# Optimization experiments

Hardware: AMD Instinct MI355X
Metric: run time of the kernel (lower is better)

## Reference

```python
import jax, jax.numpy as jnp
import numpy as np

ITEM_NUM = 1_000_000
MAXLEN = 200
H = 128
NH = 2
NB = 2
B = 2048
FLOAT_MIN = -1000.0
EPS = 1e-8


def _ln(x, g, b):
    mu = jnp.mean(x, axis=-1, keepdims=True)
    var = jnp.mean((x - mu) ** 2, axis=-1, keepdims=True)
    return (x - mu) / jnp.sqrt(var + EPS) * g + b


def setup_inputs() -> dict:
    key = jax.random.key(0)
    ks = jax.random.split(key, 32)
    s = 1.0 / np.sqrt(H)
    d = {}
    d['user_ids'] = jax.random.randint(ks[0], (B,), 0, 100000)
    d['log_seqs'] = jax.random.randint(ks[1], (B, MAXLEN), 0, ITEM_NUM)
    d['pos_seqs'] = jax.random.randint(ks[2], (B, MAXLEN), 0, ITEM_NUM)
    d['neg_seqs'] = jax.random.randint(ks[3], (B, MAXLEN), 0, ITEM_NUM)
    item = jax.random.normal(ks[4], (ITEM_NUM + 1, H), jnp.float32) * 0.02
    d['item_table'] = item.at[0].set(0.0)  # padding_idx=0
    pos = jax.random.normal(ks[5], (MAXLEN + 1, H), jnp.float32) * 0.02
    d['pos_table'] = pos.at[0].set(0.0)
    # per-block stacked params, torch Linear layout [out,in]
    d['qw'] = jax.random.normal(ks[6], (NB, H, H), jnp.float32) * s
    d['kw'] = jax.random.normal(ks[7], (NB, H, H), jnp.float32) * s
    d['vw'] = jax.random.normal(ks[8], (NB, H, H), jnp.float32) * s
    d['ow'] = jax.random.normal(ks[9], (NB, H, H), jnp.float32) * s
    d['qb'] = jnp.zeros((NB, H), jnp.float32)
    d['kb'] = jnp.zeros((NB, H), jnp.float32)
    d['vb'] = jnp.zeros((NB, H), jnp.float32)
    d['ob'] = jnp.zeros((NB, H), jnp.float32)
    d['w1'] = jax.random.normal(ks[10], (NB, H, H), jnp.float32) * s  # conv1 k=1 == linear
    d['b1'] = jnp.zeros((NB, H), jnp.float32)
    d['w2'] = jax.random.normal(ks[11], (NB, H, H), jnp.float32) * s
    d['b2'] = jnp.zeros((NB, H), jnp.float32)
    d['ln1_g'] = jnp.ones((NB, H), jnp.float32)
    d['ln1_b'] = jnp.zeros((NB, H), jnp.float32)
    d['ln2_g'] = jnp.ones((NB, H), jnp.float32)
    d['ln2_b'] = jnp.zeros((NB, H), jnp.float32)
    d['lnf_g'] = jnp.ones((H,), jnp.float32)
    d['lnf_b'] = jnp.zeros((H,), jnp.float32)
    return d


def reference(item_table, pos_table, qw, qb, kw, kb, vw, vb, ow, ob,
              ln1_g, ln1_b, w1, b1, w2, b2, ln2_g, ln2_b, lnf_g, lnf_b,
              user_ids, log_seqs, pos_seqs, neg_seqs):
    Bb, L = log_seqs.shape
    hd = H // NH
    seqs = item_table[log_seqs] * jnp.asarray(np.sqrt(H), jnp.float32)  # [B,L,H]
    poss = jnp.arange(1, L + 1)[None, :] * (log_seqs != 0)
    seqs = seqs + pos_table[poss]
    causal = jnp.triu(jnp.ones((L, L), bool), k=1)  # True = masked (future)
    for i in range(NB):
        x = seqs
        Q = (x @ qw[i].T + qb[i]).reshape(Bb, L, NH, hd).transpose(0, 2, 1, 3)
        K = (x @ kw[i].T + kb[i]).reshape(Bb, L, NH, hd).transpose(0, 2, 1, 3)
        V = (x @ vw[i].T + vb[i]).reshape(Bb, L, NH, hd).transpose(0, 2, 1, 3)
        scores = jnp.einsum('bhqd,bhkd->bhqk', Q, K) / jnp.asarray(np.sqrt(hd), jnp.float32)
        scores = jnp.where(causal, FLOAT_MIN, scores)
        attn_w = jax.nn.softmax(scores, axis=-1)
        attn = jnp.einsum('bhqk,bhkd->bhqd', attn_w, V)
        attn = attn.transpose(0, 2, 1, 3).reshape(Bb, L, H)
        mha = attn @ ow[i].T + ob[i]
        seqs = _ln(x + mha, ln1_g[i], ln1_b[i])
        ff = jax.nn.relu(seqs @ w1[i].T + b1[i]) @ w2[i].T + b2[i]
        seqs = _ln(seqs + ff, ln2_g[i], ln2_b[i])
    log_feats = _ln(seqs, lnf_g, lnf_b)
    pos_logits = jnp.sum(log_feats * item_table[pos_seqs], axis=-1)
    neg_logits = jnp.sum(log_feats * item_table[neg_seqs], axis=-1)
    return (pos_logits, neg_logits)
```

## Files before the change

### kernel.cpp

```cpp
#include <hip/hip_runtime.h>
#include <math.h>

#define L 200
#define H 128
#define HD 64
#define NB 2
#define BTOT 2048
#define HH (H * H)
#define XSS 136

typedef short bf16x8 __attribute__((ext_vector_type(8)));
typedef float f32x4 __attribute__((ext_vector_type(4)));
typedef unsigned short u16;

#define MFMA16 __builtin_amdgcn_mfma_f32_16x16x32_bf16

__device__ __forceinline__ float wsum(float v) {
#pragma unroll
    for (int off = 1; off < 64; off <<= 1) v += __shfl_xor(v, off);
    return v;
}
__device__ __forceinline__ u16 f2bf(float f) {
    unsigned u = __builtin_bit_cast(unsigned, f);
    u = u + 0x7fffu + ((u >> 16) & 1u);
    return (u16)(u >> 16);
}
__device__ __forceinline__ bf16x8 pack8(float4 a, float4 b, float sc) {
    bf16x8 r;
    r[0] = (short)f2bf(a.x * sc); r[1] = (short)f2bf(a.y * sc);
    r[2] = (short)f2bf(a.z * sc); r[3] = (short)f2bf(a.w * sc);
    r[4] = (short)f2bf(b.x * sc); r[5] = (short)f2bf(b.y * sc);
    r[6] = (short)f2bf(b.z * sc); r[7] = (short)f2bf(b.w * sc);
    return r;
}

__global__ __launch_bounds__(256) void cvt_kernel(const float* __restrict__ src,
                                                  u16* __restrict__ dst, int n8) {
    int i = blockIdx.x * 256 + threadIdx.x;
    if (i >= n8) return;
    float4 a0 = ((const float4*)src)[i * 2];
    float4 a1 = ((const float4*)src)[i * 2 + 1];
    ((bf16x8*)dst)[i] = pack8(a0, a1, 1.0f);
}

__global__ __launch_bounds__(256) void embed_kernel(const int* __restrict__ ids,
                                                    const float4* __restrict__ item,
                                                    const float4* __restrict__ post,
                                                    float4* __restrict__ X, int M) {
    int idx = blockIdx.x * 256 + threadIdx.x;
    if (idx >= M * 32) return;
    int r = idx >> 5, c = idx & 31;
    int id = ids[r];
    int l = r % L;
    int p = (id != 0) ? (l + 1) : 0;
    float4 it = item[(size_t)id * 32 + c];
    float4 pt = post[(size_t)p * 32 + c];
    const float sc = 11.313708498984761f;
    float4 o;
    o.x = it.x * sc + pt.x;
    o.y = it.y * sc + pt.y;
    o.z = it.z * sc + pt.z;
    o.w = it.w * sc + pt.w;
    X[(size_t)r * 32 + c] = o;
}

__global__ __launch_bounds__(256) void qkv_kernel(const float* __restrict__ X,
        const u16* __restrict__ wq, const u16* __restrict__ wk, const u16* __restrict__ wv,
        const float* __restrict__ qb, const float* __restrict__ kb, const float* __restrict__ vb,
        u16* __restrict__ Qo, u16* __restrict__ Ko, u16* __restrict__ Vo, int M) {
    __shared__ u16 Xs[128 * XSS];
    __shared__ u16 Ot[4][16 * XSS];
    int tid = threadIdx.x, w = tid >> 6, lane = tid & 63, g = lane >> 4, l15 = lane & 15;
    int row0 = blockIdx.x * 128;
#pragma unroll
    for (int it = 0; it < 8; ++it) {
        int idx = it * 256 + tid;
        int r = idx >> 4, c8 = idx & 15;
        size_t gr = (size_t)min(row0 + r, M - 1);
        float4 a0 = ((const float4*)X)[gr * 32 + c8 * 2];
        float4 a1 = ((const float4*)X)[gr * 32 + c8 * 2 + 1];
        *(bf16x8*)&Xs[r * XSS + c8 * 8] = pack8(a0, a1, 1.0f);
    }
    __syncthreads();

    int arow = w * 32 + l15;
    int ko = g * 8;

#pragma unroll
    for (int p = 0; p < 3; ++p) {
        const u16* Wp = p == 0 ? wq : (p == 1 ? wk : wv);
        const float* bp = p == 0 ? qb : (p == 1 ? kb : vb);
        u16* Op = p == 0 ? Qo : (p == 1 ? Ko : Vo);
        const float scale = p == 0 ? 0.125f : 1.0f;

        f32x4 acc[2][8];
#pragma unroll
        for (int nt = 0; nt < 8; ++nt) {
            float bv = bp[nt * 16 + l15];
            acc[0][nt] = (f32x4){bv, bv, bv, bv};
            acc[1][nt] = (f32x4){bv, bv, bv, bv};
        }
#pragma unroll
        for (int kc = 0; kc < 4; ++kc) {
            bf16x8 a0 = *(const bf16x8*)&Xs[arow * XSS + kc * 32 + ko];
            bf16x8 a1 = *(const bf16x8*)&Xs[(arow + 16) * XSS + kc * 32 + ko];
#pragma unroll
            for (int nt = 0; nt < 8; ++nt) {
                bf16x8 b = *(const bf16x8*)(Wp + ((size_t)(nt * 16 + l15) << 7) + kc * 32 + ko);
                acc[0][nt] = MFMA16(a0, b, acc[0][nt], 0, 0, 0);
                acc[1][nt] = MFMA16(a1, b, acc[1][nt], 0, 0, 0);
            }
        }
#pragma unroll
        for (int mt = 0; mt < 2; ++mt) {
#pragma unroll
            for (int r = 0; r < 4; ++r) {
                int ml = g * 4 + r;
#pragma unroll
                for (int nt = 0; nt < 8; ++nt)
                    Ot[w][ml * XSS + nt * 16 + l15] = f2bf(acc[mt][nt][r] * scale);
            }
            asm volatile("s_waitcnt lgkmcnt(0)" ::: "memory");
#pragma unroll
            for (int j = 0; j < 4; ++j) {
                int chunk = j * 64 + lane;
                int rr = chunk >> 4, c16 = chunk & 15;
                bf16x8 v = *(const bf16x8*)&Ot[w][rr * XSS + c16 * 8];
                int grow = row0 + w * 32 + mt * 16 + rr;
                if (grow < M) *(bf16x8*)(Op + (size_t)grow * 128 + c16 * 8) = v;
            }
            asm volatile("s_waitcnt lgkmcnt(0)" ::: "memory");
        }
    }
}

__global__ __launch_bounds__(256) void oproj_ln_kernel(const u16* __restrict__ A,
        const u16* __restrict__ W, const float* __restrict__ bias,
        const float* __restrict__ Xres, const float* __restrict__ gma,
        const float* __restrict__ bta, float* __restrict__ Y, int M) {
    int tid = threadIdx.x, w = tid >> 6, lane = tid & 63, g = lane >> 4, l15 = lane & 15;
    int row0 = blockIdx.x * 128 + w * 32;
    size_t ar0 = (size_t)min(row0 + l15, M - 1) * 128;
    size_t ar1 = (size_t)min(row0 + 16 + l15, M - 1) * 128;
    int ko = g * 8;

    f32x4 acc[2][8];
#pragma unroll
    for (int nt = 0; nt < 8; ++nt) {
        float bv = bias[nt * 16 + l15];
        acc[0][nt] = (f32x4){bv, bv, bv, bv};
        acc[1][nt] = (f32x4){bv, bv, bv, bv};
    }
#pragma unroll
    for (int kc = 0; kc < 4; ++kc) {
        bf16x8 a0 = *(const bf16x8*)(A + ar0 + kc * 32 + ko);
        bf16x8 a1 = *(const bf16x8*)(A + ar1 + kc * 32 + ko);
#pragma unroll
        for (int nt = 0; nt < 8; ++nt) {
            bf16x8 b = *(const bf16x8*)(W + ((size_t)(nt * 16 + l15) << 7) + kc * 32 + ko);
            acc[0][nt] = MFMA16(a0, b, acc[0][nt], 0, 0, 0);
            acc[1][nt] = MFMA16(a1, b, acc[1][nt], 0, 0, 0);
        }
    }
    float gg[8], bb[8];
#pragma unroll
    for (int nt = 0; nt < 8; ++nt) { gg[nt] = gma[nt * 16 + l15]; bb[nt] = bta[nt * 16 + l15]; }
#pragma unroll
    for (int mt = 0; mt < 2; ++mt) {
#pragma unroll
        for (int r = 0; r < 4; ++r) {
            int row = row0 + mt * 16 + g * 4 + r;
            size_t rb = (size_t)min(row, M - 1) * 128;
            float v[8];
            float s = 0.f;
#pragma unroll
            for (int nt = 0; nt < 8; ++nt) { v[nt] = acc[mt][nt][r] + Xres[rb + nt * 16 + l15]; s += v[nt]; }
            s += __shfl_xor(s, 1); s += __shfl_xor(s, 2); s += __shfl_xor(s, 4); s += __shfl_xor(s, 8);
            float mean = s * 0.0078125f;
            float s2 = 0.f;
#pragma unroll
            for (int nt = 0; nt < 8; ++nt) { float d = v[nt] - mean; s2 += d * d; }
            s2 += __shfl_xor(s2, 1); s2 += __shfl_xor(s2, 2); s2 += __shfl_xor(s2, 4); s2 += __shfl_xor(s2, 8);
            float inv = rsqrtf(s2 * 0.0078125f + 1e-8f);
            if (row < M) {
#pragma unroll
                for (int nt = 0; nt < 8; ++nt)
                    Y[(size_t)row * 128 + nt * 16 + l15] = (v[nt] - mean) * inv * gg[nt] + bb[nt];
            }
        }
    }
}

__global__ __launch_bounds__(256) void ffn1_kernel(const float* __restrict__ X,
        const u16* __restrict__ W, const float* __restrict__ bias,
        u16* __restrict__ Y, int M) {
    __shared__ u16 Ot[4][16 * XSS];
    int tid = threadIdx.x, w = tid >> 6, lane = tid & 63, g = lane >> 4, l15 = lane & 15;
    int row0 = blockIdx.x * 128;
    size_t ar0 = (size_t)min(row0 + w * 32 + l15, M - 1) * 32;
    size_t ar1 = (size_t)min(row0 + w * 32 + 16 + l15, M - 1) * 32;
    int ko = g * 8;

    f32x4 acc[2][8];
#pragma unroll
    for (int nt = 0; nt < 8; ++nt) {
        float bv = bias[nt * 16 + l15];
        acc[0][nt] = (f32x4){bv, bv, bv, bv};
        acc[1][nt] = (f32x4){bv, bv, bv, bv};
    }
#pragma unroll
    for (int kc = 0; kc < 4; ++kc) {
        float4 x0 = ((const float4*)X)[ar0 + kc * 8 + g * 2];
        float4 x1 = ((const float4*)X)[ar0 + kc * 8 + g * 2 + 1];
        float4 x2 = ((const float4*)X)[ar1 + kc * 8 + g * 2];
        float4 x3 = ((const float4*)X)[ar1 + kc * 8 + g * 2 + 1];
        bf16x8 a0 = pack8(x0, x1, 1.0f);
        bf16x8 a1 = pack8(x2, x3, 1.0f);
#pragma unroll
        for (int nt = 0; nt < 8; ++nt) {
            bf16x8 b = *(const bf16x8*)(W + ((size_t)(nt * 16 + l15) << 7) + kc * 32 + ko);
            acc[0][nt] = MFMA16(a0, b, acc[0][nt], 0, 0, 0);
            acc[1][nt] = MFMA16(a1, b, acc[1][nt], 0, 0, 0);
        }
    }
#pragma unroll
    for (int mt = 0; mt < 2; ++mt) {
#pragma unroll
        for (int r = 0; r < 4; ++r) {
            int ml = g * 4 + r;
#pragma unroll
            for (int nt = 0; nt < 8; ++nt)
                Ot[w][ml * XSS + nt * 16 + l15] = f2bf(fmaxf(acc[mt][nt][r], 0.f));
        }
        asm volatile("s_waitcnt lgkmcnt(0)" ::: "memory");
#pragma unroll
        for (int j = 0; j < 4; ++j) {
            int chunk = j * 64 + lane;
            int rr = chunk >> 4, c16 = chunk & 15;
            bf16x8 v = *(const bf16x8*)&Ot[w][rr * XSS + c16 * 8];
            int grow = row0 + w * 32 + mt * 16 + rr;
            if (grow < M) *(bf16x8*)(Y + (size_t)grow * 128 + c16 * 8) = v;
        }
        asm volatile("s_waitcnt lgkmcnt(0)" ::: "memory");
    }
}

__global__ __launch_bounds__(256) void ffn2_ln_kernel(const u16* __restrict__ A,
        const u16* __restrict__ W, const float* __restrict__ bias,
        const float* __restrict__ Xres, const float* __restrict__ gma,
        const float* __restrict__ bta, const float* __restrict__ gf,
        const float* __restrict__ bf_, int fin, float* __restrict__ Y, int M) {
    int tid = threadIdx.x, w = tid >> 6, lane = tid & 63, g = lane >> 4, l15 = lane & 15;
    int row0 = blockIdx.x * 128 + w * 32;
    size_t ar0 = (size_t)min(row0 + l15, M - 1) * 128;
    size_t ar1 = (size_t)min(row0 + 16 + l15, M - 1) * 128;
    int ko = g * 8;

    f32x4 acc[2][8];
#pragma unroll
    for (int nt = 0; nt < 8; ++nt) {
        float bv = bias[nt * 16 + l15];
        acc[0][nt] = (f32x4){bv, bv, bv, bv};
        acc[1][nt] = (f32x4){bv, bv, bv, bv};
    }
#pragma unroll
    for (int kc = 0; kc < 4; ++kc) {
        bf16x8 a0 = *(const bf16x8*)(A + ar0 + kc * 32 + ko);
        bf16x8 a1 = *(const bf16x8*)(A + ar1 + kc * 32 + ko);
#pragma unroll
        for (int nt = 0; nt < 8; ++nt) {
            bf16x8 b = *(const bf16x8*)(W + ((size_t)(nt * 16 + l15) << 7) + kc * 32 + ko);
            acc[0][nt] = MFMA16(a0, b, acc[0][nt], 0, 0, 0);
            acc[1][nt] = MFMA16(a1, b, acc[1][nt], 0, 0, 0);
        }
    }
    float gg[8], bb[8], gg2[8], bb2[8];
#pragma unroll
    for (int nt = 0; nt < 8; ++nt) {
        gg[nt] = gma[nt * 16 + l15]; bb[nt] = bta[nt * 16 + l15];
        gg2[nt] = gf[nt * 16 + l15]; bb2[nt] = bf_[nt * 16 + l15];
    }
#pragma unroll
    for (int mt = 0; mt < 2; ++mt) {
#pragma unroll
        for (int r = 0; r < 4; ++r) {
            int row = row0 + mt * 16 + g * 4 + r;
            size_t rb = (size_t)min(row, M - 1) * 128;
            float v[8];
            float s = 0.f;
#pragma unroll
            for (int nt = 0; nt < 8; ++nt) { v[nt] = acc[mt][nt][r] + Xres[rb + nt * 16 + l15]; s += v[nt]; }
            s += __shfl_xor(s, 1); s += __shfl_xor(s, 2); s += __shfl_xor(s, 4); s += __shfl_xor(s, 8);
            float mean = s * 0.0078125f;
            float s2 = 0.f;
#pragma unroll
            for (int nt = 0; nt < 8; ++nt) { float d = v[nt] - mean; s2 += d * d; }
            s2 += __shfl_xor(s2, 1); s2 += __shfl_xor(s2, 2); s2 += __shfl_xor(s2, 4); s2 += __shfl_xor(s2, 8);
            float inv = rsqrtf(s2 * 0.0078125f + 1e-8f);
#pragma unroll
            for (int nt = 0; nt < 8; ++nt) v[nt] = (v[nt] - mean) * inv * gg[nt] + bb[nt];
            if (fin) {
                float t = 0.f;
#pragma unroll
                for (int nt = 0; nt < 8; ++nt) t += v[nt];
                t += __shfl_xor(t, 1); t += __shfl_xor(t, 2); t += __shfl_xor(t, 4); t += __shfl_xor(t, 8);
                float mean2 = t * 0.0078125f;
                float t2 = 0.f;
#pragma unroll
                for (int nt = 0; nt < 8; ++nt) { float d = v[nt] - mean2; t2 += d * d; }
                t2 += __shfl_xor(t2, 1); t2 += __shfl_xor(t2, 2); t2 += __shfl_xor(t2, 4); t2 += __shfl_xor(t2, 8);
                float inv2 = rsqrtf(t2 * 0.0078125f + 1e-8f);
#pragma unroll
                for (int nt = 0; nt < 8; ++nt) v[nt] = (v[nt] - mean2) * inv2 * gg2[nt] + bb2[nt];
            }
            if (row < M) {
#pragma unroll
                for (int nt = 0; nt < 8; ++nt)
                    Y[(size_t)row * 128 + nt * 16 + l15] = v[nt];
            }
        }
    }
}

__global__ __launch_bounds__(256, 2) void attn_mfma_kernel(u16* __restrict__ Q,
                                                           const u16* __restrict__ K,
                                                           const u16* __restrict__ V) {
    __shared__ u16 lds_s[64 * 264];
    int b = blockIdx.x >> 1;
    int h = blockIdx.x & 1;
    int tid = threadIdx.x;
    int w = tid >> 6;
    int lane = tid & 63;
    int g = lane >> 4;
    int l15 = lane & 15;

    const u16* Kb = K + ((size_t)b * L) * H + h * HD;
    const u16* Vb = V + ((size_t)b * L) * H + h * HD;
    u16* Qb = Q + ((size_t)b * L) * H + h * HD;

    {
        int d = tid & 63;
        int kq = tid >> 6;
#pragma unroll 8
        for (int it = 0; it < 64; ++it) {
            int k = it * 4 + kq;
            lds_s[d * 264 + k] = Vb[(size_t)min(k, L - 1) * H + d];
        }
    }

    bf16x8 qf[4][2];
    int qrow[4];
#pragma unroll
    for (int nt = 0; nt < 4; ++nt) {
        int q = nt * 64 + w * 16 + l15;
        qrow[nt] = q;
        const u16* src = Qb + (size_t)min(q, L - 1) * H;
        qf[nt][0] = *(const bf16x8*)(src + g * 8);
        qf[nt][1] = *(const bf16x8*)(src + 32 + g * 8);
    }
    __syncthreads();

    f32x4 o[4][4];
    float mrun[4], lrun[4];
#pragma unroll
    for (int i = 0; i < 4; ++i) {
        mrun[i] = -1e30f; lrun[i] = 0.f;
#pragma unroll
        for (int j = 0; j < 4; ++j) o[i][j] = (f32x4){0.f, 0.f, 0.f, 0.f};
    }

    int rp = 8 * (l15 >> 2) + (l15 & 3);
    const f32x4 czero = {0.f, 0.f, 0.f, 0.f};

#pragma unroll
    for (int kc = 0; kc < 4; ++kc) {
        int kbase = kc * 64;
        bf16x8 ka[4][2];
#pragma unroll
        for (int mt = 0; mt < 4; ++mt) {
            int krow = kbase + (mt >> 1) * 32 + (mt & 1) * 4 + rp;
            const u16* src = Kb + (size_t)min(krow, L - 1) * H;
            ka[mt][0] = *(const bf16x8*)(src + g * 8);
            ka[mt][1] = *(const bf16x8*)(src + 32 + g * 8);
        }
#pragma unroll
        for (int nt = 0; nt < 4; ++nt) {
            if (nt < kc) continue;
            int q = qrow[nt];
            f32x4 c[4];
#pragma unroll
            for (int mt = 0; mt < 4; ++mt) {
                c[mt] = MFMA16(ka[mt][0], qf[nt][0], czero, 0, 0, 0);
                c[mt] = MFMA16(ka[mt][1], qf[nt][1], c[mt], 0, 0, 0);
            }
            float pm = -1e30f;
#pragma unroll
            for (int mt = 0; mt < 4; ++mt) {
#pragma unroll
                for (int r = 0; r < 4; ++r) {
                    int kact = kbase + 32 * (mt >> 1) + 4 * (mt & 1) + 8 * g + r;
                    float s = (kact <= q) ? c[mt][r] : -1e30f;
                    c[mt][r] = s;
                    pm = fmaxf(pm, s);
                }
            }
            pm = fmaxf(pm, __shfl_xor(pm, 16));
            pm = fmaxf(pm, __shfl_xor(pm, 32));
            float mnew = fmaxf(mrun[nt], pm);
            float sf = __expf(mrun[nt] - mnew);
            mrun[nt] = mnew;
            float ps = 0.f;
#pragma unroll
            for (int mt = 0; mt < 4; ++mt) {
#pragma unroll
                for (int r = 0; r < 4; ++r) {
                    float p = __expf(c[mt][r] - mnew);
                    c[mt][r] = p;
                    ps += p;
                }
            }
            ps += __shfl_xor(ps, 16);
            ps += __shfl_xor(ps, 32);
            lrun[nt] = lrun[nt] * sf + ps;
#pragma unroll
            for (int md = 0; md < 4; ++md) {
#pragma unroll
                for (int r = 0; r < 4; ++r) o[md][nt][r] *= sf;
            }
#pragma unroll
            for (int ks = 0; ks < 2; ++ks) {
                bf16x8 pb;
#pragma unroll
                for (int j = 0; j < 8; ++j)
                    pb[j] = (short)f2bf(c[2 * ks + (j >> 2)][j & 3]);
#pragma unroll
                for (int md = 0; md < 4; ++md) {
                    const u16* vp = &lds_s[(md * 16 + l15) * 264 + kbase + ks * 32 + g * 8];
                    bf16x8 va = *(const bf16x8*)vp;
                    o[md][nt] = MFMA16(va, pb, o[md][nt], 0, 0, 0);
                }
            }
        }
    }

    __syncthreads();
    u16* Ot = lds_s;
#pragma unroll
    for (int nt = 0; nt < 4; ++nt) {
        float inv = 1.0f / lrun[nt];
        int q = qrow[nt];
        int sw = (q & 7) << 3;
#pragma unroll
        for (int md = 0; md < 4; ++md) {
            int d0 = md * 16 + g * 4;
            unsigned p0 = (unsigned)f2bf(o[md][nt][0] * inv) | ((unsigned)f2bf(o[md][nt][1] * inv) << 16);
            unsigned p1 = (unsigned)f2bf(o[md][nt][2] * inv) | ((unsigned)f2bf(o[md][nt][3] * inv) << 16);
            uint2 u; u.x = p0; u.y = p1;
            *(uint2*)&Ot[q * 64 + (d0 ^ sw)] = u;
        }
    }
    __syncthreads();
    {
        int d = tid & 63;
        for (int q = tid >> 6; q < L; q += 4)
            Qb[(size_t)q * H + d] = Ot[q * 64 + (d ^ ((q & 7) << 3))];
    }
}

__global__ __launch_bounds__(256) void logits_kernel(const float* __restrict__ F,
                                                     const float* __restrict__ item,
                                                     const int* __restrict__ pid,
                                                     const int* __restrict__ nid,
                                                     float* __restrict__ out, int rows, int gofs) {
    int row = blockIdx.x * 4 + (threadIdx.x >> 6);
    int lane = threadIdx.x & 63;
    if (row >= rows) return;
    size_t base = (size_t)row * H;
    float f0 = F[base + lane], f1 = F[base + 64 + lane];
    int gr = gofs + row;
    const float* ip = item + (size_t)pid[gr] * H;
    const float* inn = item + (size_t)nid[gr] * H;
    float pv = wsum(f0 * ip[lane] + f1 * ip[lane + 64]);
    float nv = wsum(f0 * inn[lane] + f1 * inn[lane + 64]);
    if (lane == 0) {
        out[gr] = pv;
        out[(size_t)BTOT * L + gr] = nv;
    }
}

extern "C" void kernel_launch(void* const* d_in, const int* in_sizes, int n_in,
                              void* d_out, int out_size, void* d_ws, size_t ws_size,
                              hipStream_t stream) {
    const int* log_seqs = (const int*)d_in[1];
    const int* pos_seqs = (const int*)d_in[2];
    const int* neg_seqs = (const int*)d_in[3];
    const float* item = (const float*)d_in[4];
    const float* post = (const float*)d_in[5];
    const float* qw = (const float*)d_in[6];
    const float* kw = (const float*)d_in[7];
    const float* vw = (const float*)d_in[8];
    const float* ow = (const float*)d_in[9];
    const float* qb = (const float*)d_in[10];
    const float* kb = (const float*)d_in[11];
    const float* vb = (const float*)d_in[12];
    const float* ob = (const float*)d_in[13];
    const float* w1 = (const float*)d_in[14];
    const float* b1 = (const float*)d_in[15];
    const float* w2 = (const float*)d_in[16];
    const float* b2 = (const float*)d_in[17];
    const float* ln1g = (const float*)d_in[18];
    const float* ln1b = (const float*)d_in[19];
    const float* ln2g = (const float*)d_in[20];
    const float* ln2b = (const float*)d_in[21];
    const float* lnfg = (const float*)d_in[22];
    const float* lnfb = (const float*)d_in[23];
    float* out = (float*)d_out;

    int cb = BTOT;
    while (cb > 8 && (size_t)cb * L * H * 10 + 12 * HH * 2 > ws_size) cb >>= 1;
    size_t nbe = (size_t)cb * L * H;
    float* X = (float*)d_ws;
    u16* Q16 = (u16*)(X + nbe);
    u16* K16 = Q16 + nbe;
    u16* V16 = K16 + nbe;
    u16* w16 = V16 + nbe;

    const float* wsrc[6] = {qw, kw, vw, ow, w1, w2};
    int n8 = NB * HH / 8;
    for (int t = 0; t < 6; ++t)
        cvt_kernel<<<(n8 + 255) / 256, 256, 0, stream>>>(wsrc[t], w16 + (size_t)t * NB * HH, n8);

    for (int b0 = 0; b0 < BTOT; b0 += cb) {
        int M = cb * L;
        int gblk = (M + 127) / 128;
        embed_kernel<<<(M * 32 + 255) / 256, 256, 0, stream>>>(log_seqs + (size_t)b0 * L,
                                                               (const float4*)item, (const float4*)post,
                                                               (float4*)X, M);
        for (int i = 0; i < NB; ++i) {
            size_t wo = (size_t)i * HH;
            int bofs = i * H;
            qkv_kernel<<<gblk, 256, 0, stream>>>(X,
                    w16 + 0 * NB * HH + wo, w16 + 1 * NB * HH + wo, w16 + 2 * NB * HH + wo,
                    qb + bofs, kb + bofs, vb + bofs, Q16, K16, V16, M);
            attn_mfma_kernel<<<cb * 2, 256, 0, stream>>>(Q16, K16, V16);
            oproj_ln_kernel<<<gblk, 256, 0, stream>>>(Q16, w16 + 3 * NB * HH + wo, ob + bofs,
                    X, ln1g + bofs, ln1b + bofs, X, M);
            ffn1_kernel<<<gblk, 256, 0, stream>>>(X, w16 + 4 * NB * HH + wo, b1 + bofs, K16, M);
            ffn2_ln_kernel<<<gblk, 256, 0, stream>>>(K16, w16 + 5 * NB * HH + wo, b2 + bofs,
                    X, ln2g + bofs, ln2b + bofs, lnfg, lnfb, (i == NB - 1) ? 1 : 0, X, M);
        }
        logits_kernel<<<(M + 3) / 4, 256, 0, stream>>>(X, item, pos_seqs, neg_seqs, out, M, b0 * L);
    }
}
```

Baseline: 1.665 ms.

## Store activations in bf16, fuse oproj+FFN1 and logits into FFN2 epilogue

The residual stream X is now stored in bf16 rather than fp32, which halves its traffic through every kernel. Out-projection+LN1 is fused with FFN1 through an LDS staging tile, and the final logits dot products move into the last FFN2+LN epilogue. This removes the separate ffn1 and logits launches and their global round trips. It also sets the batch chunk to 512, so the sequence runs as several chunks, and accepts bf16 rounding of the residual, which may reduce accuracy.

```diff
diff --git a/kernel.cpp b/kernel.cpp
--- a/kernel.cpp
+++ b/kernel.cpp
@@ -15,15 +15,13 @@
 
 #define MFMA16 __builtin_amdgcn_mfma_f32_16x16x32_bf16
 
-__device__ __forceinline__ float wsum(float v) {
-#pragma unroll
-    for (int off = 1; off < 64; off <<= 1) v += __shfl_xor(v, off);
-    return v;
-}
 __device__ __forceinline__ u16 f2bf(float f) {
     unsigned u = __builtin_bit_cast(unsigned, f);
     u = u + 0x7fffu + ((u >> 16) & 1u);
     return (u16)(u >> 16);
+}
+__device__ __forceinline__ float bf2f(u16 s) {
+    return __builtin_bit_cast(float, ((unsigned)s) << 16);
 }
 __device__ __forceinline__ bf16x8 pack8(float4 a, float4 b, float sc) {
     bf16x8 r;
@@ -46,25 +44,24 @@
 __global__ __launch_bounds__(256) void embed_kernel(const int* __restrict__ ids,
                                                     const float4* __restrict__ item,
                                                     const float4* __restrict__ post,
-                                                    float4* __restrict__ X, int M) {
+                                                    u16* __restrict__ X, int M) {
     int idx = blockIdx.x * 256 + threadIdx.x;
-    if (idx >= M * 32) return;
-    int r = idx >> 5, c = idx & 31;
+    if (idx >= M * 16) return;
+    int r = idx >> 4, c8 = idx & 15;
     int id = ids[r];
     int l = r % L;
     int p = (id != 0) ? (l + 1) : 0;
-    float4 it = item[(size_t)id * 32 + c];
-    float4 pt = post[(size_t)p * 32 + c];
+    float4 a0 = item[(size_t)id * 32 + c8 * 2];
+    float4 a1 = item[(size_t)id * 32 + c8 * 2 + 1];
+    float4 p0 = post[(size_t)p * 32 + c8 * 2];
+    float4 p1 = post[(size_t)p * 32 + c8 * 2 + 1];
     const float sc = 11.313708498984761f;
-    float4 o;
-    o.x = it.x * sc + pt.x;
-    o.y = it.y * sc + pt.y;
-    o.z = it.z * sc + pt.z;
-    o.w = it.w * sc + pt.w;
-    X[(size_t)r * 32 + c] = o;
-}
-
-__global__ __launch_bounds__(256) void qkv_kernel(const float* __restrict__ X,
+    float4 o0 = make_float4(a0.x * sc + p0.x, a0.y * sc + p0.y, a0.z * sc + p0.z, a0.w * sc + p0.w);
+    float4 o1 = make_float4(a1.x * sc + p1.x, a1.y * sc + p1.y, a1.z * sc + p1.z, a1.w * sc + p1.w);
+    *(bf16x8*)&X[(size_t)r * 128 + c8 * 8] = pack8(o0, o1, 1.0f);
+}
+
+__global__ __launch_bounds__(256) void qkv_kernel(const u16* __restrict__ X,
         const u16* __restrict__ wq, const u16* __restrict__ wk, const u16* __restrict__ wv,
         const float* __restrict__ qb, const float* __restrict__ kb, const float* __restrict__ vb,
         u16* __restrict__ Qo, u16* __restrict__ Ko, u16* __restrict__ Vo, int M) {
@@ -77,9 +74,7 @@
         int idx = it * 256 + tid;
         int r = idx >> 4, c8 = idx & 15;
         size_t gr = (size_t)min(row0 + r, M - 1);
-        float4 a0 = ((const float4*)X)[gr * 32 + c8 * 2];
-        float4 a1 = ((const float4*)X)[gr * 32 + c8 * 2 + 1];
-        *(bf16x8*)&Xs[r * XSS + c8 * 8] = pack8(a0, a1, 1.0f);
+        *(bf16x8*)&Xs[r * XSS + c8 * 8] = *(const bf16x8*)(X + gr * 128 + c8 * 8);
     }
     __syncthreads();
 
@@ -134,20 +129,24 @@
     }
 }
 
-__global__ __launch_bounds__(256) void oproj_ln_kernel(const u16* __restrict__ A,
-        const u16* __restrict__ W, const float* __restrict__ bias,
-        const float* __restrict__ Xres, const float* __restrict__ gma,
-        const float* __restrict__ bta, float* __restrict__ Y, int M) {
+__global__ __launch_bounds__(256) void oproj_ffn1_kernel(const u16* __restrict__ A,
+        const u16* __restrict__ Wo, const float* __restrict__ ob,
+        const u16* __restrict__ Xres, const float* __restrict__ gma, const float* __restrict__ bta,
+        const u16* __restrict__ W1, const float* __restrict__ b1f,
+        u16* __restrict__ Xout, u16* __restrict__ F1, int M) {
+    __shared__ u16 Xs[128 * XSS];
+    __shared__ u16 Ot[4][16 * XSS];
     int tid = threadIdx.x, w = tid >> 6, lane = tid & 63, g = lane >> 4, l15 = lane & 15;
-    int row0 = blockIdx.x * 128 + w * 32;
-    size_t ar0 = (size_t)min(row0 + l15, M - 1) * 128;
-    size_t ar1 = (size_t)min(row0 + 16 + l15, M - 1) * 128;
+    int row0 = blockIdx.x * 128;
+    int rw = row0 + w * 32;
+    size_t ar0 = (size_t)min(rw + l15, M - 1) * 128;
+    size_t ar1 = (size_t)min(rw + 16 + l15, M - 1) * 128;
     int ko = g * 8;
 
     f32x4 acc[2][8];
 #pragma unroll
     for (int nt = 0; nt < 8; ++nt) {
-        float bv = bias[nt * 16 + l15];
+        float bv = ob[nt * 16 + l15];
         acc[0][nt] = (f32x4){bv, bv, bv, bv};
         acc[1][nt] = (f32x4){bv, bv, bv, bv};
     }
@@ -157,7 +156,7 @@
         bf16x8 a1 = *(const bf16x8*)(A + ar1 + kc * 32 + ko);
 #pragma unroll
         for (int nt = 0; nt < 8; ++nt) {
-            bf16x8 b = *(const bf16x8*)(W + ((size_t)(nt * 16 + l15) << 7) + kc * 32 + ko);
+            bf16x8 b = *(const bf16x8*)(Wo + ((size_t)(nt * 16 + l15) << 7) + kc * 32 + ko);
             acc[0][nt] = MFMA16(a0, b, acc[0][nt], 0, 0, 0);
             acc[1][nt] = MFMA16(a1, b, acc[1][nt], 0, 0, 0);
         }
@@ -169,12 +168,12 @@
     for (int mt = 0; mt < 2; ++mt) {
 #pragma unroll
         for (int r = 0; r < 4; ++r) {
-            int row = row0 + mt * 16 + g * 4 + r;
-            size_t rb = (size_t)min(row, M - 1) * 128;
+            int rowl = w * 32 + mt * 16 + g * 4 + r;
+            size_t rb = (size_t)min(row0 + rowl, M - 1) * 128;
             float v[8];
             float s = 0.f;
 #pragma unroll
-            for (int nt = 0; nt < 8; ++nt) { v[nt] = acc[mt][nt][r] + Xres[rb + nt * 16 + l15]; s += v[nt]; }
+            for (int nt = 0; nt < 8; ++nt) { v[nt] = acc[mt][nt][r] + bf2f(Xres[rb + nt * 16 + l15]); s += v[nt]; }
             s += __shfl_xor(s, 1); s += __shfl_xor(s, 2); s += __shfl_xor(s, 4); s += __shfl_xor(s, 8);
             float mean = s * 0.0078125f;
             float s2 = 0.f;
@@ -182,45 +181,39 @@
             for (int nt = 0; nt < 8; ++nt) { float d = v[nt] - mean; s2 += d * d; }
             s2 += __shfl_xor(s2, 1); s2 += __shfl_xor(s2, 2); s2 += __shfl_xor(s2, 4); s2 += __shfl_xor(s2, 8);
             float inv = rsqrtf(s2 * 0.0078125f + 1e-8f);
-            if (row < M) {
-#pragma unroll
-                for (int nt = 0; nt < 8; ++nt)
-                    Y[(size_t)row * 128 + nt * 16 + l15] = (v[nt] - mean) * inv * gg[nt] + bb[nt];
-            }
-        }
-    }
-}
-
-__global__ __launch_bounds__(256) void ffn1_kernel(const float* __restrict__ X,
-        const u16* __restrict__ W, const float* __restrict__ bias,
-        u16* __restrict__ Y, int M) {
-    __shared__ u16 Ot[4][16 * XSS];
-    int tid = threadIdx.x, w = tid >> 6, lane = tid & 63, g = lane >> 4, l15 = lane & 15;
-    int row0 = blockIdx.x * 128;
-    size_t ar0 = (size_t)min(row0 + w * 32 + l15, M - 1) * 32;
-    size_t ar1 = (size_t)min(row0 + w * 32 + 16 + l15, M - 1) * 32;
-    int ko = g * 8;
-
-    f32x4 acc[2][8];
+#pragma unroll
+            for (int nt = 0; nt < 8; ++nt)
+                Xs[rowl * XSS + nt * 16 + l15] = f2bf((v[nt] - mean) * inv * gg[nt] + bb[nt]);
+        }
+    }
+    __syncthreads();
+
+#pragma unroll
+    for (int it = 0; it < 8; ++it) {
+        int idx = it * 256 + tid;
+        int r = idx >> 4, c8 = idx & 15;
+        int grow = row0 + r;
+        if (grow < M)
+            *(bf16x8*)(Xout + (size_t)grow * 128 + c8 * 8) = *(const bf16x8*)&Xs[r * XSS + c8 * 8];
+    }
+
+    int arow = w * 32 + l15;
+    f32x4 acc2[2][8];
 #pragma unroll
     for (int nt = 0; nt < 8; ++nt) {
-        float bv = bias[nt * 16 + l15];
-        acc[0][nt] = (f32x4){bv, bv, bv, bv};
-        acc[1][nt] = (f32x4){bv, bv, bv, bv};
+        float bv = b1f[nt * 16 + l15];
+        acc2[0][nt] = (f32x4){bv, bv, bv, bv};
+        acc2[1][nt] = (f32x4){bv, bv, bv, bv};
     }
 #pragma unroll
     for (int kc = 0; kc < 4; ++kc) {
-        float4 x0 = ((const float4*)X)[ar0 + kc * 8 + g * 2];
-        float4 x1 = ((const float4*)X)[ar0 + kc * 8 + g * 2 + 1];
-        float4 x2 = ((const float4*)X)[ar1 + kc * 8 + g * 2];
-        float4 x3 = ((const float4*)X)[ar1 + kc * 8 + g * 2 + 1];
-        bf16x8 a0 = pack8(x0, x1, 1.0f);
-        bf16x8 a1 = pack8(x2, x3, 1.0f);
+        bf16x8 a0 = *(const bf16x8*)&Xs[arow * XSS + kc * 32 + ko];
+        bf16x8 a1 = *(const bf16x8*)&Xs[(arow + 16) * XSS + kc * 32 + ko];
 #pragma unroll
         for (int nt = 0; nt < 8; ++nt) {
-            bf16x8 b = *(const bf16x8*)(W + ((size_t)(nt * 16 + l15) << 7) + kc * 32 + ko);
-            acc[0][nt] = MFMA16(a0, b, acc[0][nt], 0, 0, 0);
-            acc[1][nt] = MFMA16(a1, b, acc[1][nt], 0, 0, 0);
+            bf16x8 b = *(const bf16x8*)(W1 + ((size_t)(nt * 16 + l15) << 7) + kc * 32 + ko);
+            acc2[0][nt] = MFMA16(a0, b, acc2[0][nt], 0, 0, 0);
+            acc2[1][nt] = MFMA16(a1, b, acc2[1][nt], 0, 0, 0);
         }
     }
 #pragma unroll
@@ -230,7 +223,7 @@
             int ml = g * 4 + r;
 #pragma unroll
             for (int nt = 0; nt < 8; ++nt)
-                Ot[w][ml * XSS + nt * 16 + l15] = f2bf(fmaxf(acc[mt][nt][r], 0.f));
+                Ot[w][ml * XSS + nt * 16 + l15] = f2bf(fmaxf(acc2[mt][nt][r], 0.f));
         }
         asm volatile("s_waitcnt lgkmcnt(0)" ::: "memory");
 #pragma unroll
@@ -239,21 +232,25 @@
             int rr = chunk >> 4, c16 = chunk & 15;
             bf16x8 v = *(const bf16x8*)&Ot[w][rr * XSS + c16 * 8];
             int grow = row0 + w * 32 + mt * 16 + rr;
-            if (grow < M) *(bf16x8*)(Y + (size_t)grow * 128 + c16 * 8) = v;
+            if (grow < M) *(bf16x8*)(F1 + (size_t)grow * 128 + c16 * 8) = v;
         }
         asm volatile("s_waitcnt lgkmcnt(0)" ::: "memory");
     }
 }
 
 __global__ __launch_bounds__(256) void ffn2_ln_kernel(const u16* __restrict__ A,
-        const u16* __restrict__ W, const float* __restrict__ bias,
-        const float* __restrict__ Xres, const float* __restrict__ gma,
-        const float* __restrict__ bta, const float* __restrict__ gf,
-        const float* __restrict__ bf_, int fin, float* __restrict__ Y, int M) {
+        const u16* __restrict__ W2, const float* __restrict__ bias,
+        const u16* __restrict__ Xres, const float* __restrict__ gma, const float* __restrict__ bta,
+        const float* __restrict__ gf, const float* __restrict__ bff, int fin,
+        u16* __restrict__ Xout, const float* __restrict__ item,
+        const int* __restrict__ pid, const int* __restrict__ nid,
+        float* __restrict__ out, int gofs, int M) {
+    __shared__ u16 Ot[4][16 * XSS];
     int tid = threadIdx.x, w = tid >> 6, lane = tid & 63, g = lane >> 4, l15 = lane & 15;
-    int row0 = blockIdx.x * 128 + w * 32;
-    size_t ar0 = (size_t)min(row0 + l15, M - 1) * 128;
-    size_t ar1 = (size_t)min(row0 + 16 + l15, M - 1) * 128;
+    int row0 = blockIdx.x * 128;
+    int rw = row0 + w * 32;
+    size_t ar0 = (size_t)min(rw + l15, M - 1) * 128;
+    size_t ar1 = (size_t)min(rw + 16 + l15, M - 1) * 128;
     int ko = g * 8;
 
     f32x4 acc[2][8];
@@ -269,7 +266,7 @@
         bf16x8 a1 = *(const bf16x8*)(A + ar1 + kc * 32 + ko);
 #pragma unroll
         for (int nt = 0; nt < 8; ++nt) {
-            bf16x8 b = *(const bf16x8*)(W + ((size_t)(nt * 16 + l15) << 7) + kc * 32 + ko);
+            bf16x8 b = *(const bf16x8*)(W2 + ((size_t)(nt * 16 + l15) << 7) + kc * 32 + ko);
             acc[0][nt] = MFMA16(a0, b, acc[0][nt], 0, 0, 0);
             acc[1][nt] = MFMA16(a1, b, acc[1][nt], 0, 0, 0);
         }
@@ -278,18 +275,18 @@
 #pragma unroll
     for (int nt = 0; nt < 8; ++nt) {
         gg[nt] = gma[nt * 16 + l15]; bb[nt] = bta[nt * 16 + l15];
-        gg2[nt] = gf[nt * 16 + l15]; bb2[nt] = bf_[nt * 16 + l15];
+        gg2[nt] = gf[nt * 16 + l15]; bb2[nt] = bff[nt * 16 + l15];
     }
 #pragma unroll
     for (int mt = 0; mt < 2; ++mt) {
 #pragma unroll
         for (int r = 0; r < 4; ++r) {
-            int row = row0 + mt * 16 + g * 4 + r;
+            int row = row0 + w * 32 + mt * 16 + g * 4 + r;
             size_t rb = (size_t)min(row, M - 1) * 128;
             float v[8];
             float s = 0.f;
 #pragma unroll
-            for (int nt = 0; nt < 8; ++nt) { v[nt] = acc[mt][nt][r] + Xres[rb + nt * 16 + l15]; s += v[nt]; }
+            for (int nt = 0; nt < 8; ++nt) { v[nt] = acc[mt][nt][r] + bf2f(Xres[rb + nt * 16 + l15]); s += v[nt]; }
             s += __shfl_xor(s, 1); s += __shfl_xor(s, 2); s += __shfl_xor(s, 4); s += __shfl_xor(s, 8);
             float mean = s * 0.0078125f;
             float s2 = 0.f;
@@ -312,12 +309,39 @@
                 float inv2 = rsqrtf(t2 * 0.0078125f + 1e-8f);
 #pragma unroll
                 for (int nt = 0; nt < 8; ++nt) v[nt] = (v[nt] - mean2) * inv2 * gg2[nt] + bb2[nt];
-            }
-            if (row < M) {
+                int gr = gofs + row;
+                const float* prow = item + (size_t)pid[gr] * 128;
+                const float* nrow = item + (size_t)nid[gr] * 128;
+                float sp = 0.f, sn = 0.f;
+#pragma unroll
+                for (int nt = 0; nt < 8; ++nt) {
+                    sp += v[nt] * prow[nt * 16 + l15];
+                    sn += v[nt] * nrow[nt * 16 + l15];
+                }
+                sp += __shfl_xor(sp, 1); sp += __shfl_xor(sp, 2); sp += __shfl_xor(sp, 4); sp += __shfl_xor(sp, 8);
+                sn += __shfl_xor(sn, 1); sn += __shfl_xor(sn, 2); sn += __shfl_xor(sn, 4); sn += __shfl_xor(sn, 8);
+                if (l15 == 0 && row < M) {
+                    out[gr] = sp;
+                    out[(size_t)BTOT * L + gr] = sn;
+                }
+            } else {
+                int ml = g * 4 + r;
 #pragma unroll
                 for (int nt = 0; nt < 8; ++nt)
-                    Y[(size_t)row * 128 + nt * 16 + l15] = v[nt];
-            }
+                    Ot[w][ml * XSS + nt * 16 + l15] = f2bf(v[nt]);
+            }
+        }
+        if (!fin) {
+            asm volatile("s_waitcnt lgkmcnt(0)" ::: "memory");
+#pragma unroll
+            for (int j = 0; j < 4; ++j) {
+                int chunk = j * 64 + lane;
+                int rr = chunk >> 4, c16 = chunk & 15;
+                bf16x8 v = *(const bf16x8*)&Ot[w][rr * XSS + c16 * 8];
+                int grow = row0 + w * 32 + mt * 16 + rr;
+                if (grow < M) *(bf16x8*)(Xout + (size_t)grow * 128 + c16 * 8) = v;
+            }
+            asm volatile("s_waitcnt lgkmcnt(0)" ::: "memory");
         }
     }
 }
@@ -464,27 +488,6 @@
         int d = tid & 63;
         for (int q = tid >> 6; q < L; q += 4)
             Qb[(size_t)q * H + d] = Ot[q * 64 + (d ^ ((q & 7) << 3))];
-    }
-}
-
-__global__ __launch_bounds__(256) void logits_kernel(const float* __restrict__ F,
-                                                     const float* __restrict__ item,
-                                                     const int* __restrict__ pid,
-                                                     const int* __restrict__ nid,
-                                                     float* __restrict__ out, int rows, int gofs) {
-    int row = blockIdx.x * 4 + (threadIdx.x >> 6);
-    int lane = threadIdx.x & 63;
-    if (row >= rows) return;
-    size_t base = (size_t)row * H;
-    float f0 = F[base + lane], f1 = F[base + 64 + lane];
-    int gr = gofs + row;
-    const float* ip = item + (size_t)pid[gr] * H;
-    const float* inn = item + (size_t)nid[gr] * H;
-    float pv = wsum(f0 * ip[lane] + f1 * ip[lane + 64]);
-    float nv = wsum(f0 * inn[lane] + f1 * inn[lane + 64]);
-    if (lane == 0) {
-        out[gr] = pv;
-        out[(size_t)BTOT * L + gr] = nv;
     }
 }
 
@@ -516,11 +519,11 @@
     const float* lnfb = (const float*)d_in[23];
     float* out = (float*)d_out;
 
-    int cb = BTOT;
-    while (cb > 8 && (size_t)cb * L * H * 10 + 12 * HH * 2 > ws_size) cb >>= 1;
+    int cb = 512;
+    while (cb > 8 && (size_t)cb * L * H * 8 + 12 * HH * 2 > ws_size) cb >>= 1;
     size_t nbe = (size_t)cb * L * H;
-    float* X = (float*)d_ws;
-    u16* Q16 = (u16*)(X + nbe);
+    u16* X16 = (u16*)d_ws;
+    u16* Q16 = X16 + nbe;
     u16* K16 = Q16 + nbe;
     u16* V16 = K16 + nbe;
     u16* w16 = V16 + nbe;
@@ -533,22 +536,22 @@
     for (int b0 = 0; b0 < BTOT; b0 += cb) {
         int M = cb * L;
         int gblk = (M + 127) / 128;
-        embed_kernel<<<(M * 32 + 255) / 256, 256, 0, stream>>>(log_seqs + (size_t)b0 * L,
+        embed_kernel<<<(M * 16 + 255) / 256, 256, 0, stream>>>(log_seqs + (size_t)b0 * L,
                                                                (const float4*)item, (const float4*)post,
-                                                               (float4*)X, M);
+                                                               X16, M);
         for (int i = 0; i < NB; ++i) {
             size_t wo = (size_t)i * HH;
             int bofs = i * H;
-            qkv_kernel<<<gblk, 256, 0, stream>>>(X,
+            qkv_kernel<<<gblk, 256, 0, stream>>>(X16,
                     w16 + 0 * NB * HH + wo, w16 + 1 * NB * HH + wo, w16 + 2 * NB * HH + wo,
                     qb + bofs, kb + bofs, vb + bofs, Q16, K16, V16, M);
             attn_mfma_kernel<<<cb * 2, 256, 0, stream>>>(Q16, K16, V16);
-            oproj_ln_kernel<<<gblk, 256, 0, stream>>>(Q16, w16 + 3 * NB * HH + wo, ob + bofs,
-                    X, ln1g + bofs, ln1b + bofs, X, M);
-            ffn1_kernel<<<gblk, 256, 0, stream>>>(X, w16 + 4 * NB * HH + wo, b1 + bofs, K16, M);
+            oproj_ffn1_kernel<<<gblk, 256, 0, stream>>>(Q16, w16 + 3 * NB * HH + wo, ob + bofs,
+                    X16, ln1g + bofs, ln1b + bofs,
+                    w16 + 4 * NB * HH + wo, b1 + bofs, X16, K16, M);
             ffn2_ln_kernel<<<gblk, 256, 0, stream>>>(K16, w16 + 5 * NB * HH + wo, b2 + bofs,
-                    X, ln2g + bofs, ln2b + bofs, lnfg, lnfb, (i == NB - 1) ? 1 : 0, X, M);
-        }
-        logits_kernel<<<(M + 3) / 4, 256, 0, stream>>>(X, item, pos_seqs, neg_seqs, out, M, b0 * L);
-    }
-}
+                    X16, ln2g + bofs, ln2b + bofs, lnfg, lnfb, (i == NB - 1) ? 1 : 0,
+                    X16, item, pos_seqs, neg_seqs, out, b0 * L, M);
+        }
+    }
+}
```

Measured after the change: 1.605 ms. 1.04x faster.
